# Performance work log

Measured on AMD Instinct MI355X. Metric: run time of the kernel, lower is better.

## Reference

```python
import jax, jax.numpy as jnp
import numpy as np

M, B, S = 8, 64, 1024
I = K = V = 256
H = 8
F = 1024


def setup_inputs() -> dict:
    key0 = jax.random.key(0)
    ks = iter(jax.random.split(key0, 64))
    nrm = lambda shp, s=1.0: jax.random.normal(next(ks), shp, dtype=jnp.float32) * s
    w = 0.05
    inp = {
        's0': nrm((M, B, I)), 'q0': nrm((M, B, K)), 'k0': nrm((M, B, K)), 'v0': nrm((M, B, V)),
        'key': nrm((S, B, K)), 'value': nrm((S, B, V)),
        'attn_wq': nrm((M, K, K), w), 'attn_wk': nrm((M, K, K), w), 'attn_wv': nrm((M, K, K), w),
        'attn_bq': nrm((M, K), w), 'attn_bk': nrm((M, K), w), 'attn_bv': nrm((M, K), w),
        'attn_wo': nrm((M, K, K), w), 'attn_bo': nrm((M, K), w),
    }
    for p, out in (('q', K), ('k', K), ('v', V), ('s', I)):
        inp[p + '_w1'] = nrm((M, 2 * I, F), w)
        inp[p + '_b1'] = nrm((M, F), w)
        inp[p + '_w2'] = nrm((M, F, out), w)
        inp[p + '_b2'] = nrm((M, out), w)
    inp['g_w1'] = nrm((4, M, 2 * I, F), w)
    inp['g_b1'] = nrm((4, M, F), w)
    inp['g_w2'] = nrm((4, M, F, 1), w)
    inp['g_b2'] = nrm((4, M, 1), w)
    return inp


def _forward(s0, q0, k0, v0, key, value,
             attn_wq, attn_wk, attn_wv, attn_bq, attn_bk, attn_bv, attn_wo, attn_bo,
             q_w1, q_b1, q_w2, q_b2, k_w1, k_b1, k_w2, k_b2,
             v_w1, v_b1, v_w2, v_b2, s_w1, s_b1, s_w2, s_b2,
             g_w1, g_b1, g_w2, g_b2):
    m, b, kd = q0.shape
    s = key.shape[0]
    hd = kd // H
    # per-module projections (single-query decode-style attention)
    q = jnp.einsum('mbk,mkd->mbd', q0, attn_wq) + attn_bq[:, None, :]          # (M,B,K)
    kk = jnp.einsum('sbk,mkd->msbd', key, attn_wk) + attn_bk[:, None, None, :]  # (M,S,B,K)
    vv = jnp.einsum('sbk,mkd->msbd', value, attn_wv) + attn_bv[:, None, None, :]
    qh = q.reshape(m, b, H, hd)
    kh = kk.reshape(m, s, b, H, hd)
    vh = vv.reshape(m, s, b, H, hd)
    scores = jnp.einsum('mbhd,msbhd->mbhs', qh, kh) / jnp.sqrt(jnp.float32(hd))
    aw = jax.nn.softmax(scores, axis=-1)                                        # (M,B,H,S)
    ctx = jnp.einsum('mbhs,msbhd->mbhd', aw, vh).reshape(m, b, kd)
    attn_out = jnp.einsum('mbk,mko->mbo', ctx, attn_wo) + attn_bo[:, None, :]   # (M,B,K)
    attn_weights = aw.mean(axis=2)                                              # (M,B,S)

    # _make_mlp puts ReLU FIRST: Seq(ReLU, Lin, ReLU, Lin, last_act)
    fc_in = jax.nn.relu(jnp.concatenate([attn_out, s0], axis=-1))               # (M,B,2I)

    def head(w1, b1, w2, b2):
        h = jax.nn.relu(jnp.einsum('mbi,mif->mbf', fc_in, w1) + b1[:, None, :])
        return jnp.einsum('mbf,mfo->mbo', h, w2) + b2[:, None, :]

    # non-gate heads: last activation ReLU, then .tanh() in forward
    oq = jnp.tanh(jax.nn.relu(head(q_w1, q_b1, q_w2, q_b2)))
    ok = jnp.tanh(jax.nn.relu(head(k_w1, k_b1, k_w2, k_b2)))
    ov = jnp.tanh(jax.nn.relu(head(v_w1, v_b1, v_w2, v_b2)))
    os_ = jnp.tanh(jax.nn.relu(head(s_w1, s_b1, s_w2, s_b2)))

    # gate heads stacked on leading g axis (query,key,value,state)
    gh = jax.nn.relu(jnp.einsum('mbi,gmif->gmbf', fc_in, g_w1) + g_b1[:, :, None, :])
    gates = jax.nn.sigmoid(jnp.einsum('gmbf,gmfo->gmbo', gh, g_w2) + g_b2[:, :, None, :])
    qg, kg, vg, sg = gates[0], gates[1], gates[2], gates[3]

    gq = qg * oq + (1.0 - qg) * q0
    gk = kg * ok + (1.0 - kg) * k0
    gv = vg * ov + (1.0 - vg) * v0
    gs = sg * os_ + (1.0 - sg) * s0
    return attn_out, attn_weights, gs, gq, gk, gv


def reference(s0, q0, k0, v0, key, value,
              attn_wq, attn_wk, attn_wv, attn_bq, attn_bk, attn_bv, attn_wo, attn_bo,
              q_w1, q_b1, q_w2, q_b2, k_w1, k_b1, k_w2, k_b2,
              v_w1, v_b1, v_w2, v_b2, s_w1, s_b1, s_w2, s_b2,
              g_w1, g_b1, g_w2, g_b2):
    return _forward(s0, q0, k0, v0, key, value,
                    attn_wq, attn_wk, attn_wv, attn_bq, attn_bk, attn_bv, attn_wo, attn_bo,
                    q_w1, q_b1, q_w2, q_b2, k_w1, k_b1, k_w2, k_b2,
                    v_w1, v_b1, v_w2, v_b2, s_w1, s_b1, s_w2, s_b2,
                    g_w1, g_b1, g_w2, g_b2)
```

## Files before the change

kernel.cpp:

```cpp
#include <hip/hip_runtime.h>
#include <math.h>

#define Mm 8
#define Bb 64
#define Ss 1024
#define Kk 256
#define Hh 8
#define HD 32
#define Ff 1024

typedef _Float16 f16x8 __attribute__((ext_vector_type(8)));
typedef float f32x4 __attribute__((ext_vector_type(4)));

#define WS_Q      0u
#define WS_U      131072u
#define WS_QDB    1179648u
#define WS_SC     1183744u
#define WS_W      5378048u
#define WS_H1     6426624u
#define WS_FC     0u
#define WS_GATES  262144u
#define WS_HPART  1183744u

__device__ __forceinline__ unsigned pk2(float a, float b) {
  union { unsigned u; _Float16 h[2]; } c;
  c.h[0] = (_Float16)a; c.h[1] = (_Float16)b;
  return c.u;
}

__global__ __launch_bounds__(256) void k1_qproj(
    const float* __restrict__ q0, const float* __restrict__ wq,
    const float* __restrict__ bq, float* __restrict__ qout) {
  __shared__ float q0s[8 * 260];
  const int m = blockIdx.x, b0 = blockIdx.y * 8, t = threadIdx.x;
#pragma unroll
  for (int j = 0; j < 8; ++j)
    q0s[j * 260 + t] = q0[(m * Bb + b0 + j) * Kk + t];
  __syncthreads();
  float acc[8];
  const float bias = bq[m * Kk + t];
#pragma unroll
  for (int j = 0; j < 8; ++j) acc[j] = bias;
  const float* wcol = wq + m * Kk * Kk + t;
  for (int k4 = 0; k4 < Kk / 4; ++k4) {
    const float w0 = wcol[(k4 * 4 + 0) * Kk];
    const float w1 = wcol[(k4 * 4 + 1) * Kk];
    const float w2 = wcol[(k4 * 4 + 2) * Kk];
    const float w3 = wcol[(k4 * 4 + 3) * Kk];
#pragma unroll
    for (int j = 0; j < 8; ++j) {
      const float4 qv = *(const float4*)&q0s[j * 260 + k4 * 4];
      acc[j] += qv.x * w0 + qv.y * w1 + qv.z * w2 + qv.w * w3;
    }
  }
#pragma unroll
  for (int j = 0; j < 8; ++j)
    qout[(m * Bb + b0 + j) * Kk + t] = acc[j];
}

__global__ __launch_bounds__(256) void k2_uproj(
    const float* __restrict__ wk, const float* __restrict__ bk,
    const float* __restrict__ q, float* __restrict__ u,
    float* __restrict__ qdb) {
  __shared__ float qs[64 * 36];
  const int m = blockIdx.x, h = blockIdx.y, t = threadIdx.x;
#pragma unroll
  for (int p = 0; p < 8; ++p) {
    const int idx = p * 256 + t;
    const int d = idx & 31, b = idx >> 5;
    qs[b * 36 + d] = q[(m * Bb + b) * Kk + h * HD + d];
  }
  __syncthreads();
  float acc[64];
#pragma unroll
  for (int b = 0; b < 64; ++b) acc[b] = 0.f;
  const float* wrow = wk + (m * Kk + t) * Kk + h * HD;
#pragma unroll
  for (int d4 = 0; d4 < 8; ++d4) {
    const float4 w4 = *(const float4*)&wrow[d4 * 4];
#pragma unroll
    for (int b = 0; b < 64; ++b) {
      const float4 q4 = *(const float4*)&qs[b * 36 + d4 * 4];
      acc[b] += q4.x * w4.x + q4.y * w4.y + q4.z * w4.z + q4.w * w4.w;
    }
  }
  for (int b = 0; b < 64; ++b)
    u[((m * Bb + b) * Hh + h) * Kk + t] = acc[b];
  if (t < 64) {
    float s = 0.f;
#pragma unroll
    for (int d = 0; d < 32; ++d)
      s += qs[t * 36 + d] * bk[m * Kk + h * HD + d];
    qdb[(m * Bb + t) * Hh + h] = s;
  }
}

__global__ __launch_bounds__(256) void k3_scores(
    const float* __restrict__ key, const float* __restrict__ u,
    const float* __restrict__ qdb, float* __restrict__ sc) {
  __shared__ unsigned Us[2][64 * 20];
  __shared__ unsigned Ks[2][64 * 20];
  __shared__ float qd[64];
  const int b = blockIdx.x, st0 = blockIdx.y * 64, t = threadIdx.x;
  const int w = t >> 6, lane = t & 63, quad = lane >> 4, l15 = lane & 15;
  if (t < 64) qd[t] = qdb[((t >> 3) * Bb + b) * Hh + (t & 7)];
  const int umh = t >> 2, ukg = t & 3;
  const float* ug =
      u + (((umh >> 3) * Bb + b) * Hh + (umh & 7)) * Kk + ukg * 8;
  const int ksr = t >> 2, kkg = t & 3;
  const float* kg =
      key + (size_t)(st0 + ksr) * (Bb * Kk) + b * Kk + kkg * 8;
  float4 pu[2][2], pkv[2][2];
  f32x4 acc[4];
#pragma unroll
  for (int i = 0; i < 4; ++i) acc[i] = (f32x4){0.f, 0.f, 0.f, 0.f};

#define K3_LOAD(c, s)                                   \
  {                                                     \
    pu[s][0] = *(const float4*)(ug + (c) * 32);         \
    pu[s][1] = *(const float4*)(ug + (c) * 32 + 4);     \
    pkv[s][0] = *(const float4*)(kg + (c) * 32);        \
    pkv[s][1] = *(const float4*)(kg + (c) * 32 + 4);    \
  }
#define K3_STORE(buf, s)                                                   \
  {                                                                        \
    uint4 v;                                                               \
    v.x = pk2(pu[s][0].x, pu[s][0].y); v.y = pk2(pu[s][0].z, pu[s][0].w);  \
    v.z = pk2(pu[s][1].x, pu[s][1].y); v.w = pk2(pu[s][1].z, pu[s][1].w);  \
    *(uint4*)&Us[buf][umh * 20 + ukg * 4] = v;                             \
    uint4 q_;                                                              \
    q_.x = pk2(pkv[s][0].x, pkv[s][0].y);                                  \
    q_.y = pk2(pkv[s][0].z, pkv[s][0].w);                                  \
    q_.z = pk2(pkv[s][1].x, pkv[s][1].y);                                  \
    q_.w = pk2(pkv[s][1].z, pkv[s][1].w);                                  \
    *(uint4*)&Ks[buf][ksr * 20 + kkg * 4] = q_;                            \
  }

  K3_LOAD(0, 0); K3_STORE(0, 0);
  K3_LOAD(1, 1);
#pragma unroll
  for (int c = 0; c < 8; ++c) {
    __syncthreads();
    if (c + 2 < 8) K3_LOAD(c + 2, c & 1);
    const f16x8 af = *(const f16x8*)&Us[c & 1][(w * 16 + l15) * 20 + quad * 4];
#pragma unroll
    for (int sf = 0; sf < 4; ++sf) {
      const f16x8 bf =
          *(const f16x8*)&Ks[c & 1][(sf * 16 + l15) * 20 + quad * 4];
      acc[sf] =
          __builtin_amdgcn_mfma_f32_16x16x32_f16(af, bf, acc[sf], 0, 0, 0);
    }
    if (c + 1 < 8) K3_STORE((c + 1) & 1, (c + 1) & 1);
  }
  const float scale = 0.17677669529663687f;
#pragma unroll
  for (int sf = 0; sf < 4; ++sf) {
    const int s = st0 + sf * 16 + l15;
#pragma unroll
    for (int r = 0; r < 4; ++r) {
      const int mh = w * 16 + quad * 4 + r;
      sc[(size_t)(((mh >> 3) * Bb + b) * Hh + (mh & 7)) * Ss + s] =
          (acc[sf][r] + qd[mh]) * scale;
    }
  }
#undef K3_LOAD
#undef K3_STORE
}

__global__ __launch_bounds__(256) void k3b_softmax(float* __restrict__ sc,
                                                   float* __restrict__ out) {
  __shared__ float rows[8 * 1024];
  const int m = blockIdx.x, b = blockIdx.y, t = threadIdx.x;
  const int w = t >> 6, lane = t & 63;
  const size_t base = (size_t)(m * Bb + b) * (Hh * Ss);
#pragma unroll
  for (int hh = 0; hh < 2; ++hh) {
    const int h = w * 2 + hh;
    float* g = sc + base + h * 1024;
    float4 v0 = *(const float4*)&g[lane * 4];
    float4 v1 = *(const float4*)&g[256 + lane * 4];
    float4 v2 = *(const float4*)&g[512 + lane * 4];
    float4 v3 = *(const float4*)&g[768 + lane * 4];
    float mx = fmaxf(fmaxf(fmaxf(v0.x, v0.y), fmaxf(v0.z, v0.w)),
                     fmaxf(fmaxf(v1.x, v1.y), fmaxf(v1.z, v1.w)));
    mx = fmaxf(mx, fmaxf(fmaxf(fmaxf(v2.x, v2.y), fmaxf(v2.z, v2.w)),
                         fmaxf(fmaxf(v3.x, v3.y), fmaxf(v3.z, v3.w))));
#pragma unroll
    for (int off = 32; off > 0; off >>= 1)
      mx = fmaxf(mx, __shfl_xor(mx, off, 64));
    v0.x = __expf(v0.x - mx); v0.y = __expf(v0.y - mx);
    v0.z = __expf(v0.z - mx); v0.w = __expf(v0.w - mx);
    v1.x = __expf(v1.x - mx); v1.y = __expf(v1.y - mx);
    v1.z = __expf(v1.z - mx); v1.w = __expf(v1.w - mx);
    v2.x = __expf(v2.x - mx); v2.y = __expf(v2.y - mx);
    v2.z = __expf(v2.z - mx); v2.w = __expf(v2.w - mx);
    v3.x = __expf(v3.x - mx); v3.y = __expf(v3.y - mx);
    v3.z = __expf(v3.z - mx); v3.w = __expf(v3.w - mx);
    float sm = v0.x + v0.y + v0.z + v0.w + v1.x + v1.y + v1.z + v1.w +
               v2.x + v2.y + v2.z + v2.w + v3.x + v3.y + v3.z + v3.w;
#pragma unroll
    for (int off = 32; off > 0; off >>= 1) sm += __shfl_xor(sm, off, 64);
    const float inv = 1.f / sm;
    v0.x *= inv; v0.y *= inv; v0.z *= inv; v0.w *= inv;
    v1.x *= inv; v1.y *= inv; v1.z *= inv; v1.w *= inv;
    v2.x *= inv; v2.y *= inv; v2.z *= inv; v2.w *= inv;
    v3.x *= inv; v3.y *= inv; v3.z *= inv; v3.w *= inv;
    *(float4*)&g[lane * 4] = v0;
    *(float4*)&g[256 + lane * 4] = v1;
    *(float4*)&g[512 + lane * 4] = v2;
    *(float4*)&g[768 + lane * 4] = v3;
    float* r = rows + h * 1024;
    *(float4*)&r[lane * 4] = v0;
    *(float4*)&r[256 + lane * 4] = v1;
    *(float4*)&r[512 + lane * 4] = v2;
    *(float4*)&r[768 + lane * 4] = v3;
  }
  __syncthreads();
#pragma unroll
  for (int p = 0; p < 4; ++p) {
    const int s = p * 256 + t;
    float sum = 0.f;
#pragma unroll
    for (int h = 0; h < 8; ++h) sum += rows[h * 1024 + s];
    out[131072u + (m * Bb + b) * Ss + s] = sum * 0.125f;
  }
}

__global__ __launch_bounds__(256) void k4a_av(const float* __restrict__ value,
                                              const float* __restrict__ aw,
                                              float* __restrict__ wout) {
  __shared__ unsigned Ap[2][64 * 20];
  __shared__ unsigned Vp[2][32 * 20];
  const int b = blockIdx.x, ko = blockIdx.y, t = threadIdx.x;
  const int w = t >> 6, lane = t & 63, quad = lane >> 4, l15 = lane & 15;
  const int amh = t >> 2, asg = t & 3;
  const float* ag =
      aw + ((size_t)((amh >> 3) * Bb + b) * Hh + (amh & 7)) * Ss + asg * 8;
  const int vk = (t & 15) * 2, vsp = t >> 4;
  const float* vg = value + (size_t)(2 * vsp) * (Bb * Kk) + b * Kk +
                    ko * 32 + vk;
  const size_t srow = (size_t)(Bb * Kk);
  float4 pa[2][2];
  float2 pv[2][2];
  f32x4 acc[2];
  acc[0] = (f32x4){0.f, 0.f, 0.f, 0.f};
  acc[1] = (f32x4){0.f, 0.f, 0.f, 0.f};

#define K4_LOAD(c, s)                                         \
  {                                                           \
    pa[s][0] = *(const float4*)(ag + (c) * 32);               \
    pa[s][1] = *(const float4*)(ag + (c) * 32 + 4);           \
    const float* vb = vg + (size_t)(c) * 32 * srow;           \
    pv[s][0] = *(const float2*)vb;                            \
    pv[s][1] = *(const float2*)(vb + srow);                   \
  }
#define K4_STORE(buf, s)                                                   \
  {                                                                        \
    uint4 v;                                                               \
    v.x = pk2(pa[s][0].x, pa[s][0].y); v.y = pk2(pa[s][0].z, pa[s][0].w);  \
    v.z = pk2(pa[s][1].x, pa[s][1].y); v.w = pk2(pa[s][1].z, pa[s][1].w);  \
    *(uint4*)&Ap[buf][amh * 20 + asg * 4] = v;                             \
    Vp[buf][vk * 20 + vsp] = pk2(pv[s][0].x, pv[s][1].x);                  \
    Vp[buf][(vk + 1) * 20 + vsp] = pk2(pv[s][0].y, pv[s][1].y);            \
  }

  K4_LOAD(0, 0); K4_STORE(0, 0);
  K4_LOAD(1, 1);
#pragma unroll
  for (int c = 0; c < 32; ++c) {
    __syncthreads();
    if (c + 2 < 32) K4_LOAD(c + 2, c & 1);
    const f16x8 af = *(const f16x8*)&Ap[c & 1][(w * 16 + l15) * 20 + quad * 4];
#pragma unroll
    for (int nt = 0; nt < 2; ++nt) {
      const f16x8 bf =
          *(const f16x8*)&Vp[c & 1][(nt * 16 + l15) * 20 + quad * 4];
      acc[nt] =
          __builtin_amdgcn_mfma_f32_16x16x32_f16(af, bf, acc[nt], 0, 0, 0);
    }
    if (c + 1 < 32) K4_STORE((c + 1) & 1, (c + 1) & 1);
  }
#pragma unroll
  for (int nt = 0; nt < 2; ++nt) {
    const int k = ko * 32 + nt * 16 + l15;
#pragma unroll
    for (int r = 0; r < 4; ++r) {
      const int mh = w * 16 + quad * 4 + r;
      wout[((size_t)((mh >> 3) * Bb + b) * Hh + (mh & 7)) * Kk + k] =
          acc[nt][r];
    }
  }
#undef K4_LOAD
#undef K4_STORE
}

__global__ __launch_bounds__(256) void k5_ctx(
    const float* __restrict__ wv, const float* __restrict__ bv,
    const float* __restrict__ wo, const float* __restrict__ bo,
    const float* __restrict__ s0in, const float* __restrict__ w,
    float* __restrict__ attn_out, float* __restrict__ fc) {
  __shared__ float wsh[2048];
  __shared__ float ctxs[256];
  const int m = blockIdx.x, b = blockIdx.y, t = threadIdx.x;
  const int base = (m * Bb + b) * (Hh * Kk);
#pragma unroll
  for (int p = 0; p < 8; ++p) wsh[p * 256 + t] = w[base + p * 256 + t];
  __syncthreads();
  const int h = t >> 5;
  float acc = bv[m * Kk + t];
  const float* wvc = wv + m * Kk * Kk + t;
  for (int k4 = 0; k4 < 64; ++k4) {
    const float4 a4 = *(const float4*)&wsh[h * 256 + k4 * 4];
    acc += a4.x * wvc[(k4 * 4 + 0) * Kk] + a4.y * wvc[(k4 * 4 + 1) * Kk] +
           a4.z * wvc[(k4 * 4 + 2) * Kk] + a4.w * wvc[(k4 * 4 + 3) * Kk];
  }
  ctxs[t] = acc;
  __syncthreads();
  float acc2 = bo[m * Kk + t];
  const float* woc = wo + m * Kk * Kk + t;
  for (int k4 = 0; k4 < 64; ++k4) {
    const float4 c4 = *(const float4*)&ctxs[k4 * 4];
    acc2 += c4.x * woc[(k4 * 4 + 0) * Kk] + c4.y * woc[(k4 * 4 + 1) * Kk] +
            c4.z * woc[(k4 * 4 + 2) * Kk] + c4.w * woc[(k4 * 4 + 3) * Kk];
  }
  const int ob = (m * Bb + b) * Kk + t;
  attn_out[ob] = acc2;
  fc[(m * Bb + b) * 512 + t] = fmaxf(acc2, 0.f);
  fc[(m * Bb + b) * 512 + 256 + t] = fmaxf(s0in[ob], 0.f);
}

__global__ __launch_bounds__(256) void k6_mlp1(
    const float* __restrict__ fc, const float* __restrict__ w1q,
    const float* __restrict__ w1k, const float* __restrict__ w1v,
    const float* __restrict__ w1s, const float* __restrict__ w1g,
    const float* __restrict__ b1q, const float* __restrict__ b1k,
    const float* __restrict__ b1v, const float* __restrict__ b1s,
    const float* __restrict__ b1g, float* __restrict__ h1) {
  __shared__ unsigned As[2][64 * 20];
  __shared__ unsigned Ws[2][16 * 68];
  const int ft = blockIdx.x, m = blockIdx.y, head = blockIdx.z,
            t = threadIdx.x;
  const float* w1;
  const float* b1;
  if (head == 0)      { w1 = w1q; b1 = b1q; }
  else if (head == 1) { w1 = w1k; b1 = b1k; }
  else if (head == 2) { w1 = w1v; b1 = b1v; }
  else if (head == 3) { w1 = w1s; b1 = b1s; }
  else {
    w1 = w1g + (size_t)(head - 4) * (Mm * 512 * Ff);
    b1 = b1g + (head - 4) * (Mm * Ff);
  }
  w1 += (size_t)m * 512 * Ff;
  b1 += m * Ff;
  const int w = t >> 6, lane = t & 63, quad = lane >> 4, l15 = lane & 15;
  const int abb = t >> 2, akg = t & 3;
  const float* ag = fc + (m * Bb + abb) * 512 + akg * 8;
  const int wf0 = (t & 15) * 4, wkp = t >> 4;
  const float* wg = w1 + (size_t)(2 * wkp) * Ff + ft * 64 + wf0;
  float4 pa[2][2], pw[2][2];
  f32x4 acc[4];
#pragma unroll
  for (int i = 0; i < 4; ++i) acc[i] = (f32x4){0.f, 0.f, 0.f, 0.f};

#define K6_LOAD(c, s)                                            \
  {                                                              \
    pa[s][0] = *(const float4*)(ag + (c) * 32);                  \
    pa[s][1] = *(const float4*)(ag + (c) * 32 + 4);              \
    const float* wb = wg + (size_t)(c) * 32 * Ff;                \
    pw[s][0] = *(const float4*)wb;                               \
    pw[s][1] = *(const float4*)(wb + Ff);                        \
  }
#define K6_STORE(buf, s)                                                   \
  {                                                                        \
    uint4 v;                                                               \
    v.x = pk2(pa[s][0].x, pa[s][0].y); v.y = pk2(pa[s][0].z, pa[s][0].w);  \
    v.z = pk2(pa[s][1].x, pa[s][1].y); v.w = pk2(pa[s][1].z, pa[s][1].w);  \
    *(uint4*)&As[buf][abb * 20 + akg * 4] = v;                             \
    uint4 wv_;                                                             \
    wv_.x = pk2(pw[s][0].x, pw[s][1].x);                                   \
    wv_.y = pk2(pw[s][0].y, pw[s][1].y);                                   \
    wv_.z = pk2(pw[s][0].z, pw[s][1].z);                                   \
    wv_.w = pk2(pw[s][0].w, pw[s][1].w);                                   \
    *(uint4*)&Ws[buf][wkp * 68 + wf0] = wv_;                               \
  }

  K6_LOAD(0, 0); K6_STORE(0, 0);
  K6_LOAD(1, 1);
#pragma unroll
  for (int c = 0; c < 16; ++c) {
    __syncthreads();
    if (c + 2 < 16) K6_LOAD(c + 2, c & 1);
    union { f16x8 v; unsigned u[4]; } bfu;
#pragma unroll
    for (int j = 0; j < 4; ++j)
      bfu.u[j] = Ws[c & 1][(quad * 4 + j) * 68 + w * 16 + l15];
    const f16x8 bf = bfu.v;
#pragma unroll
    for (int mt = 0; mt < 4; ++mt) {
      const f16x8 af =
          *(const f16x8*)&As[c & 1][(mt * 16 + l15) * 20 + quad * 4];
      acc[mt] =
          __builtin_amdgcn_mfma_f32_16x16x32_f16(af, bf, acc[mt], 0, 0, 0);
    }
    if (c + 1 < 16) K6_STORE((c + 1) & 1, (c + 1) & 1);
  }
  const int f = ft * 64 + w * 16 + l15;
  const float bias = b1[f];
  float* hb = h1 + (size_t)((head * Mm + m) * Bb) * Ff + f;
#pragma unroll
  for (int mt = 0; mt < 4; ++mt) {
#pragma unroll
    for (int r = 0; r < 4; ++r) {
      const int bb = mt * 16 + quad * 4 + r;
      hb[(size_t)bb * Ff] = fmaxf(acc[mt][r] + bias, 0.f);
    }
  }
#undef K6_LOAD
#undef K6_STORE
}

__global__ __launch_bounds__(64) void k6b_gates(
    const float* __restrict__ h1, const float* __restrict__ gw2,
    const float* __restrict__ gb2, float* __restrict__ gates) {
  const int gm = blockIdx.x, b = blockIdx.y, t = threadIdx.x;
  const int g = gm >> 3, m = gm & 7;
  const float* hrow = h1 + (size_t)(((4 + g) * Mm + m) * Bb + b) * Ff;
  const float* wrow = gw2 + (g * Mm + m) * Ff;
  float s = 0.f;
#pragma unroll
  for (int i = 0; i < 16; ++i) s += hrow[t + i * 64] * wrow[t + i * 64];
  for (int off = 32; off > 0; off >>= 1) s += __shfl_down(s, off, 64);
  if (t == 0)
    gates[(g * Mm + m) * Bb + b] =
        1.f / (1.f + __expf(-(s + gb2[g * Mm + m])));
}

__global__ __launch_bounds__(256) void k7a_mlp2(
    const float* __restrict__ h1, const float* __restrict__ w2q,
    const float* __restrict__ w2k, const float* __restrict__ w2v,
    const float* __restrict__ w2s, float* __restrict__ hpart) {
  __shared__ unsigned As[2][64 * 20];
  __shared__ unsigned Ws[2][16 * 68];
  const int ot = blockIdx.x & 3, fq = blockIdx.x >> 2;
  const int m = blockIdx.y, head = blockIdx.z, t = threadIdx.x;
  const float* w2 =
      (head == 0) ? w2q : (head == 1) ? w2k : (head == 2) ? w2v : w2s;
  w2 += (size_t)m * Ff * Kk;
  const int w = t >> 6, lane = t & 63, quad = lane >> 4, l15 = lane & 15;
  const int abb = t >> 2, akg = t & 3;
  const float* ag =
      h1 + (size_t)((head * Mm + m) * Bb + abb) * Ff + fq * 256 + akg * 8;
  const int wf0 = (t & 15) * 4, wkp = t >> 4;
  const float* wg = w2 + (size_t)(fq * 256 + 2 * wkp) * Kk + ot * 64 + wf0;
  float4 pa[2][2], pw[2][2];
  f32x4 acc[4];
#pragma unroll
  for (int i = 0; i < 4; ++i) acc[i] = (f32x4){0.f, 0.f, 0.f, 0.f};

#define K7_LOAD(c, s)                                            \
  {                                                              \
    pa[s][0] = *(const float4*)(ag + (c) * 32);                  \
    pa[s][1] = *(const float4*)(ag + (c) * 32 + 4);              \
    const float* wb = wg + (size_t)(c) * 32 * Kk;                \
    pw[s][0] = *(const float4*)wb;                               \
    pw[s][1] = *(const float4*)(wb + Kk);                        \
  }
#define K7_STORE(buf, s)                                                   \
  {                                                                        \
    uint4 v;                                                               \
    v.x = pk2(pa[s][0].x, pa[s][0].y); v.y = pk2(pa[s][0].z, pa[s][0].w);  \
    v.z = pk2(pa[s][1].x, pa[s][1].y); v.w = pk2(pa[s][1].z, pa[s][1].w);  \
    *(uint4*)&As[buf][abb * 20 + akg * 4] = v;                             \
    uint4 wv_;                                                             \
    wv_.x = pk2(pw[s][0].x, pw[s][1].x);                                   \
    wv_.y = pk2(pw[s][0].y, pw[s][1].y);                                   \
    wv_.z = pk2(pw[s][0].z, pw[s][1].z);                                   \
    wv_.w = pk2(pw[s][0].w, pw[s][1].w);                                   \
    *(uint4*)&Ws[buf][wkp * 68 + wf0] = wv_;                               \
  }

  K7_LOAD(0, 0); K7_STORE(0, 0);
  K7_LOAD(1, 1);
#pragma unroll
  for (int c = 0; c < 8; ++c) {
    __syncthreads();
    if (c + 2 < 8) K7_LOAD(c + 2, c & 1);
    union { f16x8 v; unsigned u[4]; } bfu;
#pragma unroll
    for (int j = 0; j < 4; ++j)
      bfu.u[j] = Ws[c & 1][(quad * 4 + j) * 68 + w * 16 + l15];
    const f16x8 bf = bfu.v;
#pragma unroll
    for (int mt = 0; mt < 4; ++mt) {
      const f16x8 af =
          *(const f16x8*)&As[c & 1][(mt * 16 + l15) * 20 + quad * 4];
      acc[mt] =
          __builtin_amdgcn_mfma_f32_16x16x32_f16(af, bf, acc[mt], 0, 0, 0);
    }
    if (c + 1 < 8) K7_STORE((c + 1) & 1, (c + 1) & 1);
  }
  const int o = ot * 64 + w * 16 + l15;
  float* hp =
      hpart + fq * 524288u + (size_t)((head * Mm + m) * Bb) * Kk + o;
#pragma unroll
  for (int mt = 0; mt < 4; ++mt) {
#pragma unroll
    for (int r = 0; r < 4; ++r) {
      const int bb = mt * 16 + quad * 4 + r;
      hp[(size_t)bb * Kk] = acc[mt][r];
    }
  }
#undef K7_LOAD
#undef K7_STORE
}

__global__ __launch_bounds__(256) void k7b_final(
    const float* __restrict__ hpart, const float* __restrict__ gates,
    const float* __restrict__ b2q, const float* __restrict__ b2k,
    const float* __restrict__ b2v, const float* __restrict__ b2s,
    const float* __restrict__ q0, const float* __restrict__ k0,
    const float* __restrict__ v0, const float* __restrict__ s0,
    float* __restrict__ out) {
  const int idx = blockIdx.x * 256 + threadIdx.x;
  const int o = idx & 255;
  const int b = (idx >> 8) & 63;
  const int m = (idx >> 14) & 7;
  const int head = idx >> 17;
  const float* b2 = (head == 0) ? b2q : (head == 1) ? b2k
                    : (head == 2) ? b2v : b2s;
  const float* x0 = (head == 0) ? q0 : (head == 1) ? k0
                    : (head == 2) ? v0 : s0;
  const unsigned ooff = (head == 0) ? 786432u
                        : (head == 1) ? 917504u
                        : (head == 2) ? 1048576u : 655360u;
  float v = hpart[idx] + hpart[524288u + idx] + hpart[1048576u + idx] +
            hpart[1572864u + idx] + b2[m * Kk + o];
  v = tanhf(fmaxf(v, 0.f));
  const float g = gates[(head * Mm + m) * Bb + b];
  const float x = x0[(m * Bb + b) * Kk + o];
  out[ooff + (m * Bb + b) * Kk + o] = g * v + (1.f - g) * x;
}

extern "C" void kernel_launch(void* const* d_in, const int* in_sizes, int n_in,
                              void* d_out, int out_size, void* d_ws,
                              size_t ws_size, hipStream_t stream) {
  (void)in_sizes; (void)n_in; (void)out_size; (void)ws_size;
  const float* s0  = (const float*)d_in[0];
  const float* q0  = (const float*)d_in[1];
  const float* k0  = (const float*)d_in[2];
  const float* v0  = (const float*)d_in[3];
  const float* key = (const float*)d_in[4];
  const float* val = (const float*)d_in[5];
  const float* wq  = (const float*)d_in[6];
  const float* wk  = (const float*)d_in[7];
  const float* wv  = (const float*)d_in[8];
  const float* bqa = (const float*)d_in[9];
  const float* bka = (const float*)d_in[10];
  const float* bva = (const float*)d_in[11];
  const float* wo  = (const float*)d_in[12];
  const float* bo  = (const float*)d_in[13];
  const float* qw1 = (const float*)d_in[14];
  const float* qb1 = (const float*)d_in[15];
  const float* qw2 = (const float*)d_in[16];
  const float* qb2 = (const float*)d_in[17];
  const float* kw1 = (const float*)d_in[18];
  const float* kb1 = (const float*)d_in[19];
  const float* kw2 = (const float*)d_in[20];
  const float* kb2 = (const float*)d_in[21];
  const float* vw1 = (const float*)d_in[22];
  const float* vb1 = (const float*)d_in[23];
  const float* vw2 = (const float*)d_in[24];
  const float* vb2 = (const float*)d_in[25];
  const float* sw1 = (const float*)d_in[26];
  const float* sb1 = (const float*)d_in[27];
  const float* sw2 = (const float*)d_in[28];
  const float* sb2 = (const float*)d_in[29];
  const float* gw1 = (const float*)d_in[30];
  const float* gb1 = (const float*)d_in[31];
  const float* gw2 = (const float*)d_in[32];
  const float* gb2 = (const float*)d_in[33];
  float* ws  = (float*)d_ws;
  float* out = (float*)d_out;

  k1_qproj<<<dim3(8, 8), 256, 0, stream>>>(q0, wq, bqa, ws + WS_Q);
  k2_uproj<<<dim3(8, 8), 256, 0, stream>>>(wk, bka, ws + WS_Q, ws + WS_U,
                                           ws + WS_QDB);
  k3_scores<<<dim3(64, 16), 256, 0, stream>>>(key, ws + WS_U, ws + WS_QDB,
                                              ws + WS_SC);
  k3b_softmax<<<dim3(8, 64), 256, 0, stream>>>(ws + WS_SC, out);
  k4a_av<<<dim3(64, 8), 256, 0, stream>>>(val, ws + WS_SC, ws + WS_W);
  k5_ctx<<<dim3(8, 64), 256, 0, stream>>>(wv, bva, wo, bo, s0, ws + WS_W, out,
                                          ws + WS_FC);
  k6_mlp1<<<dim3(16, 8, 8), 256, 0, stream>>>(ws + WS_FC, qw1, kw1, vw1, sw1,
                                              gw1, qb1, kb1, vb1, sb1, gb1,
                                              ws + WS_H1);
  k6b_gates<<<dim3(32, 64), 64, 0, stream>>>(ws + WS_H1, gw2, gb2,
                                             ws + WS_GATES);
  k7a_mlp2<<<dim3(16, 8, 4), 256, 0, stream>>>(ws + WS_H1, qw2, kw2, vw2, sw2,
                                               ws + WS_HPART);
  k7b_final<<<dim3(2048), 256, 0, stream>>>(ws + WS_HPART, ws + WS_GATES, qb2,
                                            kb2, vb2, sb2, q0, k0, v0, s0,
                                            out);
}
```

Baseline: 426.1 us.

## Stage GEMM tiles with direct global-to-LDS DMA and split attention-value reduction over S

The four MFMA GEMM kernels (scores, attention-value, MLP1, MLP2) now copy fp32 tiles straight from global memory into LDS with global_load_lds and an XOR swizzle. The fp16 conversion moves to fragment-read time, which removes the register staging and pack-to-LDS stores. The attention-value kernel is also split over four S-chunks with larger output tiles, so it writes partial sums that k5 adds together. The cost is twice the LDS footprint, scalar fp16 conversions inside the inner loop, and extra workspace traffic for the partial results.

New measurement: 431.3 us. Within noise of the previous version (+1.2%).

```diff
diff --git a/kernel.cpp b/kernel.cpp
--- a/kernel.cpp
+++ b/kernel.cpp
@@ -16,16 +16,42 @@
 #define WS_U      131072u
 #define WS_QDB    1179648u
 #define WS_SC     1183744u
-#define WS_W      5378048u
-#define WS_H1     6426624u
+#define WS_WPART  5378048u
 #define WS_FC     0u
+#define WS_H1     5378048u
 #define WS_GATES  262144u
 #define WS_HPART  1183744u
 
-__device__ __forceinline__ unsigned pk2(float a, float b) {
-  union { unsigned u; _Float16 h[2]; } c;
-  c.h[0] = (_Float16)a; c.h[1] = (_Float16)b;
-  return c.u;
+__device__ __forceinline__ void dma16(const float* g, float* l) {
+  __builtin_amdgcn_global_load_lds(
+      (const __attribute__((address_space(1))) unsigned int*)g,
+      (__attribute__((address_space(3))) unsigned int*)l, 16, 0, 0);
+}
+
+__device__ __forceinline__ f16x8 frag_ctg(const float* T, int r, int quad) {
+  const int x = r & 7;
+  const float4 a0 = *(const float4*)&T[r * 32 + (((2 * quad) ^ x) << 2)];
+  const float4 a1 = *(const float4*)&T[r * 32 + (((2 * quad + 1) ^ x) << 2)];
+  f16x8 f;
+  f[0] = (_Float16)a0.x; f[1] = (_Float16)a0.y;
+  f[2] = (_Float16)a0.z; f[3] = (_Float16)a0.w;
+  f[4] = (_Float16)a1.x; f[5] = (_Float16)a1.y;
+  f[6] = (_Float16)a1.z; f[7] = (_Float16)a1.w;
+  return f;
+}
+
+__device__ __forceinline__ int swz(int kr) {
+  return (kr & 15) ^ ((kr >> 3) << 1);
+}
+__device__ __forceinline__ f16x8 frag_ctr(const float* T, int col, int quad) {
+  const int g = col >> 2, c = col & 3;
+  f16x8 f;
+#pragma unroll
+  for (int j = 0; j < 8; ++j) {
+    const int kr = quad * 8 + j;
+    f[j] = (_Float16)T[kr * 64 + ((g ^ swz(kr)) << 2) + c];
+  }
+  return f;
 }
 
 __global__ __launch_bounds__(256) void k1_qproj(
@@ -98,59 +124,48 @@
 __global__ __launch_bounds__(256) void k3_scores(
     const float* __restrict__ key, const float* __restrict__ u,
     const float* __restrict__ qdb, float* __restrict__ sc) {
-  __shared__ unsigned Us[2][64 * 20];
-  __shared__ unsigned Ks[2][64 * 20];
+  __shared__ __attribute__((aligned(16))) float TA[2][2048];
+  __shared__ __attribute__((aligned(16))) float TB[2][2048];
   __shared__ float qd[64];
   const int b = blockIdx.x, st0 = blockIdx.y * 64, t = threadIdx.x;
-  const int w = t >> 6, lane = t & 63, quad = lane >> 4, l15 = lane & 15;
+  const int w = t >> 6, lane = t & 63, quad = (t >> 4) & 3, l15 = t & 15;
   if (t < 64) qd[t] = qdb[((t >> 3) * Bb + b) * Hh + (t & 7)];
-  const int umh = t >> 2, ukg = t & 3;
-  const float* ug =
-      u + (((umh >> 3) * Bb + b) * Hh + (umh & 7)) * Kk + ukg * 8;
-  const int ksr = t >> 2, kkg = t & 3;
-  const float* kg =
-      key + (size_t)(st0 + ksr) * (Bb * Kk) + b * Kk + kkg * 8;
-  float4 pu[2][2], pkv[2][2];
+
+  auto dmaAB = [&](int c, int buf) {
+#pragma unroll
+    for (int j = 0; j < 2; ++j) {
+      const int r = w * 16 + j * 8 + (lane >> 3);
+      const int gp = (lane & 7) ^ (r & 7);
+      dma16(u + (((r >> 3) * Bb + b) * Hh + (r & 7)) * Kk + c * 32 + gp * 4,
+            &TA[buf][(w * 2 + j) * 256 + lane * 4]);
+    }
+#pragma unroll
+    for (int j = 0; j < 2; ++j) {
+      const int sr = w * 16 + j * 8 + (lane >> 3);
+      const int gp = (lane & 7) ^ (sr & 7);
+      dma16(key + (size_t)(st0 + sr) * (Bb * Kk) + b * Kk + c * 32 + gp * 4,
+            &TB[buf][(w * 2 + j) * 256 + lane * 4]);
+    }
+  };
+
   f32x4 acc[4];
 #pragma unroll
   for (int i = 0; i < 4; ++i) acc[i] = (f32x4){0.f, 0.f, 0.f, 0.f};
-
-#define K3_LOAD(c, s)                                   \
-  {                                                     \
-    pu[s][0] = *(const float4*)(ug + (c) * 32);         \
-    pu[s][1] = *(const float4*)(ug + (c) * 32 + 4);     \
-    pkv[s][0] = *(const float4*)(kg + (c) * 32);        \
-    pkv[s][1] = *(const float4*)(kg + (c) * 32 + 4);    \
-  }
-#define K3_STORE(buf, s)                                                   \
-  {                                                                        \
-    uint4 v;                                                               \
-    v.x = pk2(pu[s][0].x, pu[s][0].y); v.y = pk2(pu[s][0].z, pu[s][0].w);  \
-    v.z = pk2(pu[s][1].x, pu[s][1].y); v.w = pk2(pu[s][1].z, pu[s][1].w);  \
-    *(uint4*)&Us[buf][umh * 20 + ukg * 4] = v;                             \
-    uint4 q_;                                                              \
-    q_.x = pk2(pkv[s][0].x, pkv[s][0].y);                                  \
-    q_.y = pk2(pkv[s][0].z, pkv[s][0].w);                                  \
-    q_.z = pk2(pkv[s][1].x, pkv[s][1].y);                                  \
-    q_.w = pk2(pkv[s][1].z, pkv[s][1].w);                                  \
-    *(uint4*)&Ks[buf][ksr * 20 + kkg * 4] = q_;                            \
-  }
-
-  K3_LOAD(0, 0); K3_STORE(0, 0);
-  K3_LOAD(1, 1);
+  dmaAB(0, 0);
+  __syncthreads();
 #pragma unroll
   for (int c = 0; c < 8; ++c) {
-    __syncthreads();
-    if (c + 2 < 8) K3_LOAD(c + 2, c & 1);
-    const f16x8 af = *(const f16x8*)&Us[c & 1][(w * 16 + l15) * 20 + quad * 4];
+    if (c + 1 < 8) dmaAB(c + 1, (c + 1) & 1);
+    const float* A = TA[c & 1];
+    const float* B = TB[c & 1];
+    const f16x8 af = frag_ctg(A, w * 16 + l15, quad);
 #pragma unroll
     for (int sf = 0; sf < 4; ++sf) {
-      const f16x8 bf =
-          *(const f16x8*)&Ks[c & 1][(sf * 16 + l15) * 20 + quad * 4];
+      const f16x8 bf = frag_ctg(B, sf * 16 + l15, quad);
       acc[sf] =
           __builtin_amdgcn_mfma_f32_16x16x32_f16(af, bf, acc[sf], 0, 0, 0);
     }
-    if (c + 1 < 8) K3_STORE((c + 1) & 1, (c + 1) & 1);
+    __syncthreads();
   }
   const float scale = 0.17677669529663687f;
 #pragma unroll
@@ -163,8 +178,6 @@
           (acc[sf][r] + qd[mh]) * scale;
     }
   }
-#undef K3_LOAD
-#undef K3_STORE
 }
 
 __global__ __launch_bounds__(256) void k3b_softmax(float* __restrict__ sc,
@@ -228,83 +241,78 @@
 
 __global__ __launch_bounds__(256) void k4a_av(const float* __restrict__ value,
                                               const float* __restrict__ aw,
-                                              float* __restrict__ wout) {
-  __shared__ unsigned Ap[2][64 * 20];
-  __shared__ unsigned Vp[2][32 * 20];
-  const int b = blockIdx.x, ko = blockIdx.y, t = threadIdx.x;
-  const int w = t >> 6, lane = t & 63, quad = lane >> 4, l15 = lane & 15;
-  const int amh = t >> 2, asg = t & 3;
-  const float* ag =
-      aw + ((size_t)((amh >> 3) * Bb + b) * Hh + (amh & 7)) * Ss + asg * 8;
-  const int vk = (t & 15) * 2, vsp = t >> 4;
-  const float* vg = value + (size_t)(2 * vsp) * (Bb * Kk) + b * Kk +
-                    ko * 32 + vk;
-  const size_t srow = (size_t)(Bb * Kk);
-  float4 pa[2][2];
-  float2 pv[2][2];
-  f32x4 acc[2];
-  acc[0] = (f32x4){0.f, 0.f, 0.f, 0.f};
-  acc[1] = (f32x4){0.f, 0.f, 0.f, 0.f};
-
-#define K4_LOAD(c, s)                                         \
-  {                                                           \
-    pa[s][0] = *(const float4*)(ag + (c) * 32);               \
-    pa[s][1] = *(const float4*)(ag + (c) * 32 + 4);           \
-    const float* vb = vg + (size_t)(c) * 32 * srow;           \
-    pv[s][0] = *(const float2*)vb;                            \
-    pv[s][1] = *(const float2*)(vb + srow);                   \
-  }
-#define K4_STORE(buf, s)                                                   \
-  {                                                                        \
-    uint4 v;                                                               \
-    v.x = pk2(pa[s][0].x, pa[s][0].y); v.y = pk2(pa[s][0].z, pa[s][0].w);  \
-    v.z = pk2(pa[s][1].x, pa[s][1].y); v.w = pk2(pa[s][1].z, pa[s][1].w);  \
-    *(uint4*)&Ap[buf][amh * 20 + asg * 4] = v;                             \
-    Vp[buf][vk * 20 + vsp] = pk2(pv[s][0].x, pv[s][1].x);                  \
-    Vp[buf][(vk + 1) * 20 + vsp] = pk2(pv[s][0].y, pv[s][1].y);            \
-  }
-
-  K4_LOAD(0, 0); K4_STORE(0, 0);
-  K4_LOAD(1, 1);
-#pragma unroll
-  for (int c = 0; c < 32; ++c) {
+                                              float* __restrict__ wpart) {
+  __shared__ __attribute__((aligned(16))) float TA[2][2048];
+  __shared__ __attribute__((aligned(16))) float TB[2][2048];
+  const int b = blockIdx.x, ko = blockIdx.y, sq = blockIdx.z, t = threadIdx.x;
+  const int w = t >> 6, lane = t & 63, quad = (t >> 4) & 3, l15 = t & 15;
+
+  auto dmaAB = [&](int c, int buf) {
+#pragma unroll
+    for (int j = 0; j < 2; ++j) {
+      const int r = w * 16 + j * 8 + (lane >> 3);
+      const int gp = (lane & 7) ^ (r & 7);
+      dma16(aw + ((size_t)((r >> 3) * Bb + b) * Hh + (r & 7)) * Ss +
+                sq * 256 + c * 32 + gp * 4,
+            &TA[buf][(w * 2 + j) * 256 + lane * 4]);
+    }
+#pragma unroll
+    for (int j = 0; j < 2; ++j) {
+      const int kr = w * 8 + j * 4 + (lane >> 4);
+      const int gp = (lane & 15) ^ swz(kr);
+      dma16(value + (size_t)(sq * 256 + c * 32 + kr) * (Bb * Kk) + b * Kk +
+                ko * 64 + gp * 4,
+            &TB[buf][(w * 2 + j) * 256 + lane * 4]);
+    }
+  };
+
+  f32x4 acc[4];
+#pragma unroll
+  for (int i = 0; i < 4; ++i) acc[i] = (f32x4){0.f, 0.f, 0.f, 0.f};
+  dmaAB(0, 0);
+  __syncthreads();
+#pragma unroll
+  for (int c = 0; c < 8; ++c) {
+    if (c + 1 < 8) dmaAB(c + 1, (c + 1) & 1);
+    const float* A = TA[c & 1];
+    const float* B = TB[c & 1];
+    const f16x8 af = frag_ctg(A, w * 16 + l15, quad);
+#pragma unroll
+    for (int nf = 0; nf < 4; ++nf) {
+      const f16x8 bf = frag_ctr(B, nf * 16 + l15, quad);
+      acc[nf] =
+          __builtin_amdgcn_mfma_f32_16x16x32_f16(af, bf, acc[nf], 0, 0, 0);
+    }
     __syncthreads();
-    if (c + 2 < 32) K4_LOAD(c + 2, c & 1);
-    const f16x8 af = *(const f16x8*)&Ap[c & 1][(w * 16 + l15) * 20 + quad * 4];
-#pragma unroll
-    for (int nt = 0; nt < 2; ++nt) {
-      const f16x8 bf =
-          *(const f16x8*)&Vp[c & 1][(nt * 16 + l15) * 20 + quad * 4];
-      acc[nt] =
-          __builtin_amdgcn_mfma_f32_16x16x32_f16(af, bf, acc[nt], 0, 0, 0);
-    }
-    if (c + 1 < 32) K4_STORE((c + 1) & 1, (c + 1) & 1);
-  }
-#pragma unroll
-  for (int nt = 0; nt < 2; ++nt) {
-    const int k = ko * 32 + nt * 16 + l15;
+  }
+  float* wp = wpart + sq * 1048576u;
+#pragma unroll
+  for (int nf = 0; nf < 4; ++nf) {
+    const int k = ko * 64 + nf * 16 + l15;
 #pragma unroll
     for (int r = 0; r < 4; ++r) {
       const int mh = w * 16 + quad * 4 + r;
-      wout[((size_t)((mh >> 3) * Bb + b) * Hh + (mh & 7)) * Kk + k] =
-          acc[nt][r];
-    }
-  }
-#undef K4_LOAD
-#undef K4_STORE
+      wp[((size_t)((mh >> 3) * Bb + b) * Hh + (mh & 7)) * Kk + k] =
+          acc[nf][r];
+    }
+  }
 }
 
 __global__ __launch_bounds__(256) void k5_ctx(
     const float* __restrict__ wv, const float* __restrict__ bv,
     const float* __restrict__ wo, const float* __restrict__ bo,
-    const float* __restrict__ s0in, const float* __restrict__ w,
+    const float* __restrict__ s0in, const float* __restrict__ wpart,
     float* __restrict__ attn_out, float* __restrict__ fc) {
   __shared__ float wsh[2048];
   __shared__ float ctxs[256];
   const int m = blockIdx.x, b = blockIdx.y, t = threadIdx.x;
   const int base = (m * Bb + b) * (Hh * Kk);
 #pragma unroll
-  for (int p = 0; p < 8; ++p) wsh[p * 256 + t] = w[base + p * 256 + t];
+  for (int p = 0; p < 8; ++p) {
+    const int o = base + p * 256 + t;
+    wsh[p * 256 + t] = wpart[o] + wpart[1048576u + o] + wpart[2097152u + o] +
+                       wpart[3145728u + o];
+  }
   __syncthreads();
   const int h = t >> 5;
   float acc = bv[m * Kk + t];
@@ -336,8 +344,8 @@
     const float* __restrict__ b1q, const float* __restrict__ b1k,
     const float* __restrict__ b1v, const float* __restrict__ b1s,
     const float* __restrict__ b1g, float* __restrict__ h1) {
-  __shared__ unsigned As[2][64 * 20];
-  __shared__ unsigned Ws[2][16 * 68];
+  __shared__ __attribute__((aligned(16))) float TA[2][2048];
+  __shared__ __attribute__((aligned(16))) float TB[2][2048];
   const int ft = blockIdx.x, m = blockIdx.y, head = blockIdx.z,
             t = threadIdx.x;
   const float* w1;
@@ -352,57 +360,44 @@
   }
   w1 += (size_t)m * 512 * Ff;
   b1 += m * Ff;
-  const int w = t >> 6, lane = t & 63, quad = lane >> 4, l15 = lane & 15;
-  const int abb = t >> 2, akg = t & 3;
-  const float* ag = fc + (m * Bb + abb) * 512 + akg * 8;
-  const int wf0 = (t & 15) * 4, wkp = t >> 4;
-  const float* wg = w1 + (size_t)(2 * wkp) * Ff + ft * 64 + wf0;
-  float4 pa[2][2], pw[2][2];
+  const int w = t >> 6, lane = t & 63, quad = (t >> 4) & 3, l15 = t & 15;
+  const float* fcm = fc + m * Bb * 512;
+
+  auto dmaAB = [&](int c, int buf) {
+#pragma unroll
+    for (int j = 0; j < 2; ++j) {
+      const int r = w * 16 + j * 8 + (lane >> 3);
+      const int gp = (lane & 7) ^ (r & 7);
+      dma16(fcm + r * 512 + c * 32 + gp * 4,
+            &TA[buf][(w * 2 + j) * 256 + lane * 4]);
+    }
+#pragma unroll
+    for (int j = 0; j < 2; ++j) {
+      const int kr = w * 8 + j * 4 + (lane >> 4);
+      const int gp = (lane & 15) ^ swz(kr);
+      dma16(w1 + (size_t)(c * 32 + kr) * Ff + ft * 64 + gp * 4,
+            &TB[buf][(w * 2 + j) * 256 + lane * 4]);
+    }
+  };
+
   f32x4 acc[4];
 #pragma unroll
   for (int i = 0; i < 4; ++i) acc[i] = (f32x4){0.f, 0.f, 0.f, 0.f};
-
-#define K6_LOAD(c, s)                                            \
-  {                                                              \
-    pa[s][0] = *(const float4*)(ag + (c) * 32);                  \
-    pa[s][1] = *(const float4*)(ag + (c) * 32 + 4);              \
-    const float* wb = wg + (size_t)(c) * 32 * Ff;                \
-    pw[s][0] = *(const float4*)wb;                               \
-    pw[s][1] = *(const float4*)(wb + Ff);                        \
-  }
-#define K6_STORE(buf, s)                                                   \
-  {                                                                        \
-    uint4 v;                                                               \
-    v.x = pk2(pa[s][0].x, pa[s][0].y); v.y = pk2(pa[s][0].z, pa[s][0].w);  \
-    v.z = pk2(pa[s][1].x, pa[s][1].y); v.w = pk2(pa[s][1].z, pa[s][1].w);  \
-    *(uint4*)&As[buf][abb * 20 + akg * 4] = v;                             \
-    uint4 wv_;                                                             \
-    wv_.x = pk2(pw[s][0].x, pw[s][1].x);                                   \
-    wv_.y = pk2(pw[s][0].y, pw[s][1].y);                                   \
-    wv_.z = pk2(pw[s][0].z, pw[s][1].z);                                   \
-    wv_.w = pk2(pw[s][0].w, pw[s][1].w);                                   \
-    *(uint4*)&Ws[buf][wkp * 68 + wf0] = wv_;                               \
-  }
-
-  K6_LOAD(0, 0); K6_STORE(0, 0);
-  K6_LOAD(1, 1);
+  dmaAB(0, 0);
+  __syncthreads();
 #pragma unroll
   for (int c = 0; c < 16; ++c) {
-    __syncthreads();
-    if (c + 2 < 16) K6_LOAD(c + 2, c & 1);
-    union { f16x8 v; unsigned u[4]; } bfu;
-#pragma unroll
-    for (int j = 0; j < 4; ++j)
-      bfu.u[j] = Ws[c & 1][(quad * 4 + j) * 68 + w * 16 + l15];
-    const f16x8 bf = bfu.v;
+    if (c + 1 < 16) dmaAB(c + 1, (c + 1) & 1);
+    const float* A = TA[c & 1];
+    const float* B = TB[c & 1];
+    const f16x8 bf = frag_ctr(B, w * 16 + l15, quad);
 #pragma unroll
     for (int mt = 0; mt < 4; ++mt) {
-      const f16x8 af =
-          *(const f16x8*)&As[c & 1][(mt * 16 + l15) * 20 + quad * 4];
+      const f16x8 af = frag_ctg(A, mt * 16 + l15, quad);
       acc[mt] =
           __builtin_amdgcn_mfma_f32_16x16x32_f16(af, bf, acc[mt], 0, 0, 0);
     }
-    if (c + 1 < 16) K6_STORE((c + 1) & 1, (c + 1) & 1);
+    __syncthreads();
   }
   const int f = ft * 64 + w * 16 + l15;
   const float bias = b1[f];
@@ -415,8 +410,6 @@
       hb[(size_t)bb * Ff] = fmaxf(acc[mt][r] + bias, 0.f);
     }
   }
-#undef K6_LOAD
-#undef K6_STORE
 }
 
 __global__ __launch_bounds__(64) void k6b_gates(
@@ -439,69 +432,54 @@
     const float* __restrict__ h1, const float* __restrict__ w2q,
     const float* __restrict__ w2k, const float* __restrict__ w2v,
     const float* __restrict__ w2s, float* __restrict__ hpart) {
-  __shared__ unsigned As[2][64 * 20];
-  __shared__ unsigned Ws[2][16 * 68];
+  __shared__ __attribute__((aligned(16))) float TA[2][2048];
+  __shared__ __attribute__((aligned(16))) float TB[2][2048];
   const int ot = blockIdx.x & 3, fq = blockIdx.x >> 2;
   const int m = blockIdx.y, head = blockIdx.z, t = threadIdx.x;
   const float* w2 =
       (head == 0) ? w2q : (head == 1) ? w2k : (head == 2) ? w2v : w2s;
   w2 += (size_t)m * Ff * Kk;
-  const int w = t >> 6, lane = t & 63, quad = lane >> 4, l15 = lane & 15;
-  const int abb = t >> 2, akg = t & 3;
-  const float* ag =
-      h1 + (size_t)((head * Mm + m) * Bb + abb) * Ff + fq * 256 + akg * 8;
-  const int wf0 = (t & 15) * 4, wkp = t >> 4;
-  const float* wg = w2 + (size_t)(fq * 256 + 2 * wkp) * Kk + ot * 64 + wf0;
-  float4 pa[2][2], pw[2][2];
+  const int w = t >> 6, lane = t & 63, quad = (t >> 4) & 3, l15 = t & 15;
+  const float* hbase = h1 + (size_t)((head * Mm + m) * Bb) * Ff + fq * 256;
+
+  auto dmaAB = [&](int c, int buf) {
+#pragma unroll
+    for (int j = 0; j < 2; ++j) {
+      const int r = w * 16 + j * 8 + (lane >> 3);
+      const int gp = (lane & 7) ^ (r & 7);
+      dma16(hbase + (size_t)r * Ff + c * 32 + gp * 4,
+            &TA[buf][(w * 2 + j) * 256 + lane * 4]);
+    }
+#pragma unroll
+    for (int j = 0; j < 2; ++j) {
+      const int kr = w * 8 + j * 4 + (lane >> 4);
+      const int gp = (lane & 15) ^ swz(kr);
+      dma16(w2 + (size_t)(fq * 256 + c * 32 + kr) * Kk + ot * 64 + gp * 4,
+            &TB[buf][(w * 2 + j) * 256 + lane * 4]);
+    }
+  };
+
   f32x4 acc[4];
 #pragma unroll
   for (int i = 0; i < 4; ++i) acc[i] = (f32x4){0.f, 0.f, 0.f, 0.f};
-
-#define K7_LOAD(c, s)                                            \
-  {                                                              \
-    pa[s][0] = *(const float4*)(ag + (c) * 32);                  \
-    pa[s][1] = *(const float4*)(ag + (c) * 32 + 4);              \
-    const float* wb = wg + (size_t)(c) * 32 * Kk;                \
-    pw[s][0] = *(const float4*)wb;                               \
-    pw[s][1] = *(const float4*)(wb + Kk);                        \
-  }
-#define K7_STORE(buf, s)                                                   \
-  {                                                                        \
-    uint4 v;                                                               \
-    v.x = pk2(pa[s][0].x, pa[s][0].y); v.y = pk2(pa[s][0].z, pa[s][0].w);  \
-    v.z = pk2(pa[s][1].x, pa[s][1].y); v.w = pk2(pa[s][1].z, pa[s][1].w);  \
-    *(uint4*)&As[buf][abb * 20 + akg * 4] = v;                             \
-    uint4 wv_;                                                             \
-    wv_.x = pk2(pw[s][0].x, pw[s][1].x);                                   \
-    wv_.y = pk2(pw[s][0].y, pw[s][1].y);                                   \
-    wv_.z = pk2(pw[s][0].z, pw[s][1].z);                                   \
-    wv_.w = pk2(pw[s][0].w, pw[s][1].w);                                   \
-    *(uint4*)&Ws[buf][wkp * 68 + wf0] = wv_;                               \
-  }
-
-  K7_LOAD(0, 0); K7_STORE(0, 0);
-  K7_LOAD(1, 1);
+  dmaAB(0, 0);
+  __syncthreads();
 #pragma unroll
   for (int c = 0; c < 8; ++c) {
-    __syncthreads();
-    if (c + 2 < 8) K7_LOAD(c + 2, c & 1);
-    union { f16x8 v; unsigned u[4]; } bfu;
-#pragma unroll
-    for (int j = 0; j < 4; ++j)
-      bfu.u[j] = Ws[c & 1][(quad * 4 + j) * 68 + w * 16 + l15];
-    const f16x8 bf = bfu.v;
+    if (c + 1 < 8) dmaAB(c + 1, (c + 1) & 1);
+    const float* A = TA[c & 1];
+    const float* B = TB[c & 1];
+    const f16x8 bf = frag_ctr(B, w * 16 + l15, quad);
 #pragma unroll
     for (int mt = 0; mt < 4; ++mt) {
-      const f16x8 af =
-          *(const f16x8*)&As[c & 1][(mt * 16 + l15) * 20 + quad * 4];
+      const f16x8 af = frag_ctg(A, mt * 16 + l15, quad);
       acc[mt] =
           __builtin_amdgcn_mfma_f32_16x16x32_f16(af, bf, acc[mt], 0, 0, 0);
     }
-    if (c + 1 < 8) K7_STORE((c + 1) & 1, (c + 1) & 1);
+    __syncthreads();
   }
   const int o = ot * 64 + w * 16 + l15;
-  float* hp =
-      hpart + fq * 524288u + (size_t)((head * Mm + m) * Bb) * Kk + o;
+  float* hp = hpart + fq * 524288u + (size_t)((head * Mm + m) * Bb) * Kk + o;
 #pragma unroll
   for (int mt = 0; mt < 4; ++mt) {
 #pragma unroll
@@ -510,8 +488,6 @@
       hp[(size_t)bb * Kk] = acc[mt][r];
     }
   }
-#undef K7_LOAD
-#undef K7_STORE
 }
 
 __global__ __launch_bounds__(256) void k7b_final(
@@ -588,9 +564,9 @@
   k3_scores<<<dim3(64, 16), 256, 0, stream>>>(key, ws + WS_U, ws + WS_QDB,
                                               ws + WS_SC);
   k3b_softmax<<<dim3(8, 64), 256, 0, stream>>>(ws + WS_SC, out);
-  k4a_av<<<dim3(64, 8), 256, 0, stream>>>(val, ws + WS_SC, ws + WS_W);
-  k5_ctx<<<dim3(8, 64), 256, 0, stream>>>(wv, bva, wo, bo, s0, ws + WS_W, out,
-                                          ws + WS_FC);
+  k4a_av<<<dim3(64, 4, 4), 256, 0, stream>>>(val, ws + WS_SC, ws + WS_WPART);
+  k5_ctx<<<dim3(8, 64), 256, 0, stream>>>(wv, bva, wo, bo, s0, ws + WS_WPART,
+                                          out, ws + WS_FC);
   k6_mlp1<<<dim3(16, 8, 8), 256, 0, stream>>>(ws + WS_FC, qw1, kw1, vw1, sw1,
                                               gw1, qb1, kb1, vb1, sb1, gb1,
                                               ws + WS_H1);
```
